# Kernel tuning notes

Hardware: AMD Instinct MI355X
Metric: run time of the kernel (lower is better)

The kernel has to match this reference:

```python
import jax, jax.numpy as jnp
import numpy as np

N_NODES = 500_000
N_EDGES = 32_000_000
D_COEF = 1.0  # 'd' init arg, constant


def setup_inputs() -> dict:
    key = jax.random.key(0)
    k1, k2, k3 = jax.random.split(key, 3)
    theta = jax.random.normal(k1, (N_NODES, 1), dtype=jnp.float32)
    src = jax.random.randint(k2, (N_EDGES,), 0, N_NODES, dtype=jnp.int32)
    dst = jax.random.randint(k3, (N_EDGES,), 0, N_NODES, dtype=jnp.int32)
    logc = jnp.asarray(np.log(1.5), dtype=jnp.float32)  # continuousTimeVicsek2D.logc
    u0 = jnp.asarray(0.3, dtype=jnp.float32)
    return {"theta": theta, "logc": logc, "u0": u0, "src": src, "dst": dst}


def reference(theta, logc, u0, src, dst):
    # calc_message: dtheta = theta[src] - theta[dst]; m = exp(logc)*sin(d*dtheta)
    dtheta = theta[src] - theta[dst]              # [E,1] edge gather
    msg = jnp.exp(logc) * jnp.sin(dtheta * D_COEF)  # [E,1]
    # aggregate_message: mean over each node's incoming mailbox (segment mean by dst)
    n = theta.shape[0]
    w_sum = jax.ops.segment_sum(msg, dst, num_segments=n)          # [N,1]
    cnt = jax.ops.segment_sum(jnp.ones((dst.shape[0], 1), msg.dtype), dst, num_segments=n)
    w = w_sum / jnp.maximum(cnt, 1.0)             # [N,1] torque (0 if no in-edges)
    # polarity2velocity: v = u0 * [cos(theta), sin(theta)]
    v = u0 * jnp.concatenate([jnp.cos(theta), jnp.sin(theta)], axis=-1)  # [N,2]
    # return torque and velocity concatenated: [N,3] = [w | v]
    return jnp.concatenate([w, v], axis=-1)
```

## Files before the change

### kernel.cpp

```cpp
#include <hip/hip_runtime.h>


#define NB 62
#define BSHIFT 13
#define NODES_PER_B 8192
#define CAPB 548000u
#define TPB 256
#define EPT 16
#define EPI (TPB * EPT)
#define K_SLICES 8
#define MSG_BITS 18

__global__ __launch_bounds__(TPB) void scatter_kernel(
    const float* __restrict__ theta,
    const float* __restrict__ logc,
    const int* __restrict__ src,
    const int* __restrict__ dst,
    unsigned int* __restrict__ recs,
    unsigned int* __restrict__ cursors,
    int n_edges, int n_iters)
{
    __shared__ unsigned int hist[NB];
    __shared__ unsigned int rankc[NB];
    __shared__ unsigned int offs[NB];
    __shared__ unsigned int gbase[NB];
    __shared__ unsigned int sbuf[EPI];
    __shared__ unsigned char sbkt[EPI];

    const float c = __expf(logc[0]);
    const int tid = threadIdx.x;

    for (int iter = blockIdx.x; iter < n_iters; iter += gridDim.x) {
        const int base = iter * EPI + tid * EPT;

        if (tid < NB) { hist[tid] = 0; rankc[tid] = 0; }
        __syncthreads();

        unsigned int myrec[EPT];
        int myb[EPT];

        if (base + EPT <= n_edges) {
            int4 s4[4], d4[4];
            #pragma unroll
            for (int q = 0; q < 4; ++q) {
                s4[q] = ((const int4*)(src + base))[q];
                d4[q] = ((const int4*)(dst + base))[q];
            }
            const int* sp = (const int*)s4;
            const int* dp = (const int*)d4;
            #pragma unroll
            for (int j = 0; j < EPT; ++j) {
                int dn = dp[j];
                float m = c * __sinf(theta[sp[j]] - theta[dn]);
                unsigned int a18 = (unsigned int)((m + 2.0f) * 65536.0f + 0.5f);
                myrec[j] = (((unsigned int)(dn & (NODES_PER_B - 1))) << MSG_BITS) | a18;
                int b = dn >> BSHIFT;
                myb[j] = b;
                atomicAdd(&hist[b], 1u);
            }
        } else {
            #pragma unroll
            for (int j = 0; j < EPT; ++j) {
                int e = base + j;
                if (e < n_edges) {
                    int dn = dst[e];
                    float m = c * __sinf(theta[src[e]] - theta[dn]);
                    unsigned int a18 = (unsigned int)((m + 2.0f) * 65536.0f + 0.5f);
                    myrec[j] = (((unsigned int)(dn & (NODES_PER_B - 1))) << MSG_BITS) | a18;
                    int b = dn >> BSHIFT;
                    myb[j] = b;
                    atomicAdd(&hist[b], 1u);
                } else {
                    myb[j] = -1;
                }
            }
        }
        __syncthreads();

        if (tid < 64) {
            unsigned int h = (tid < NB) ? hist[tid] : 0u;
            unsigned int x = h;
            #pragma unroll
            for (int dlt = 1; dlt < 64; dlt <<= 1) {
                unsigned int y = __shfl_up(x, dlt, 64);
                if (tid >= dlt) x += y;
            }
            if (tid < NB) {
                offs[tid] = x - h;
                gbase[tid] = h ? atomicAdd(&cursors[tid], h) : 0u;
            }
        }
        __syncthreads();

        #pragma unroll
        for (int j = 0; j < EPT; ++j) {
            int b = myb[j];
            if (b >= 0) {
                unsigned int r = atomicAdd(&rankc[b], 1u);
                unsigned int slot = offs[b] + r;
                sbuf[slot] = myrec[j];
                sbkt[slot] = (unsigned char)b;
            }
        }
        __syncthreads();

        unsigned int total = offs[NB - 1] + hist[NB - 1];
        for (unsigned int slot = tid; slot < total; slot += TPB) {
            unsigned int b = sbkt[slot];
            unsigned int gpos = gbase[b] + (slot - offs[b]);
            if (gpos < CAPB) recs[(size_t)b * CAPB + gpos] = sbuf[slot];
        }
        __syncthreads();
    }
}

__global__ __launch_bounds__(TPB) void reduce_kernel(
    const unsigned int* __restrict__ recs,
    const unsigned int* __restrict__ cursors,
    unsigned int* __restrict__ partials)
{
    __shared__ unsigned int acc[NODES_PER_B];
    const int tid = threadIdx.x;
    const int b = blockIdx.x >> 3;
    const int k = blockIdx.x & 7;

    for (int j = tid; j < NODES_PER_B; j += TPB) acc[j] = 0u;
    __syncthreads();

    unsigned int cnt = cursors[b];
    if (cnt > CAPB) cnt = CAPB;
    unsigned int slice = (cnt + K_SLICES - 1) / K_SLICES;
    unsigned int lo = (unsigned int)k * slice;
    unsigned int hi = lo + slice; if (hi > cnt) hi = cnt;

    const unsigned int* bp = recs + (size_t)b * CAPB;
    unsigned int i = lo + tid;
    for (; i + 3u * TPB < hi; i += 4u * TPB) {
        unsigned int r0 = bp[i];
        unsigned int r1 = bp[i + TPB];
        unsigned int r2 = bp[i + 2u * TPB];
        unsigned int r3 = bp[i + 3u * TPB];
        unsigned int a0 = ((r0 & 0x3FFFFu) + 2u) >> 2;
        unsigned int a1 = ((r1 & 0x3FFFFu) + 2u) >> 2;
        unsigned int a2 = ((r2 & 0x3FFFFu) + 2u) >> 2;
        unsigned int a3 = ((r3 & 0x3FFFFu) + 2u) >> 2;
        atomicAdd(&acc[r0 >> MSG_BITS], (a0 << 8) | 1u);
        atomicAdd(&acc[r1 >> MSG_BITS], (a1 << 8) | 1u);
        atomicAdd(&acc[r2 >> MSG_BITS], (a2 << 8) | 1u);
        atomicAdd(&acc[r3 >> MSG_BITS], (a3 << 8) | 1u);
    }
    for (; i < hi; i += TPB) {
        unsigned int rec = bp[i];
        unsigned int a = ((rec & 0x3FFFFu) + 2u) >> 2;
        atomicAdd(&acc[rec >> MSG_BITS], (a << 8) | 1u);
    }
    __syncthreads();

    unsigned int* pb = partials + (size_t)blockIdx.x * NODES_PER_B;
    for (int j = tid; j < NODES_PER_B; j += TPB) pb[j] = acc[j];
}

__global__ __launch_bounds__(TPB) void node_kernel(
    const float* __restrict__ theta,
    const float* __restrict__ u0p,
    const unsigned int* __restrict__ partials,
    float* __restrict__ out,
    int n_nodes)
{
    int i = blockIdx.x * TPB + threadIdx.x;
    if (i >= n_nodes) return;
    int b = i >> BSHIFT;
    int l = i & (NODES_PER_B - 1);

    unsigned int cnt = 0; int sum = 0;
    #pragma unroll
    for (int k = 0; k < K_SLICES; ++k) {
        unsigned int p = partials[(size_t)(b * K_SLICES + k) * NODES_PER_B + l];
        cnt += p & 255u;
        sum += (int)(p >> 8);
    }
    int net = sum - (int)cnt * 32768;
    float w = (float)net * (1.0f / 16384.0f) / fmaxf((float)cnt, 1.0f);

    float t = theta[i];
    float u0 = u0p[0];
    out[3 * i + 0] = w;
    out[3 * i + 1] = u0 * __cosf(t);
    out[3 * i + 2] = u0 * __sinf(t);
}

__global__ __launch_bounds__(256) void edge_kernel_fb(
    const float* __restrict__ theta, const float* __restrict__ logc,
    const int* __restrict__ src, const int* __restrict__ dst,
    unsigned long long* __restrict__ acc, int n_edges)
{
    const float c = __expf(logc[0]);
    int base = (blockIdx.x * 256 + threadIdx.x) * 4;
    if (base + 3 < n_edges) {
        int4 s4 = *(const int4*)(src + base);
        int4 d4 = *(const int4*)(dst + base);
        float m0 = c * __sinf(theta[s4.x] - theta[d4.x]);
        float m1 = c * __sinf(theta[s4.y] - theta[d4.y]);
        float m2 = c * __sinf(theta[s4.z] - theta[d4.z]);
        float m3 = c * __sinf(theta[s4.w] - theta[d4.w]);
        atomicAdd(&acc[d4.x], ((unsigned long long)((m0 + 2.0f) * 1073741824.0f) << 24) | 1ull);
        atomicAdd(&acc[d4.y], ((unsigned long long)((m1 + 2.0f) * 1073741824.0f) << 24) | 1ull);
        atomicAdd(&acc[d4.z], ((unsigned long long)((m2 + 2.0f) * 1073741824.0f) << 24) | 1ull);
        atomicAdd(&acc[d4.w], ((unsigned long long)((m3 + 2.0f) * 1073741824.0f) << 24) | 1ull);
    } else {
        for (int e = base; e < n_edges; ++e) {
            int s = src[e], d = dst[e];
            float m = c * __sinf(theta[s] - theta[d]);
            atomicAdd(&acc[d], ((unsigned long long)((m + 2.0f) * 1073741824.0f) << 24) | 1ull);
        }
    }
}

__global__ __launch_bounds__(256) void node_kernel_fb(
    const float* __restrict__ theta, const float* __restrict__ u0p,
    const unsigned long long* __restrict__ acc, float* __restrict__ out, int n_nodes)
{
    int i = blockIdx.x * 256 + threadIdx.x;
    if (i >= n_nodes) return;
    unsigned long long p = acc[i];
    long long cnt = (long long)(p & 0xFFFFFFull);
    long long net = (long long)(p >> 24) - (cnt << 31);
    float sum = (float)((double)net * (1.0 / 1073741824.0));
    float w = sum / fmaxf((float)cnt, 1.0f);
    float t = theta[i]; float u0 = u0p[0];
    out[3 * i + 0] = w;
    out[3 * i + 1] = u0 * __cosf(t);
    out[3 * i + 2] = u0 * __sinf(t);
}

extern "C" void kernel_launch(void* const* d_in, const int* in_sizes, int n_in,
                              void* d_out, int out_size, void* d_ws, size_t ws_size,
                              hipStream_t stream) {
    const float* theta = (const float*)d_in[0];
    const float* logc  = (const float*)d_in[1];
    const float* u0    = (const float*)d_in[2];
    const int*   src   = (const int*)d_in[3];
    const int*   dst   = (const int*)d_in[4];
    float* out = (float*)d_out;

    int n_nodes = in_sizes[0];
    int n_edges = in_sizes[3];

    size_t recs_bytes     = (size_t)NB * CAPB * sizeof(unsigned int);
    size_t cursors_off    = (recs_bytes + 255) & ~(size_t)255;
    size_t partials_off   = (cursors_off + 256 + 255) & ~(size_t)255;
    size_t partials_bytes = (size_t)NB * K_SLICES * NODES_PER_B * sizeof(unsigned int);
    size_t need = partials_off + partials_bytes;

    bool fast = (ws_size >= need) && (n_nodes <= NB * NODES_PER_B);

    if (fast) {
        unsigned int* recs     = (unsigned int*)d_ws;
        unsigned int* cursors  = (unsigned int*)((char*)d_ws + cursors_off);
        unsigned int* partials = (unsigned int*)((char*)d_ws + partials_off);

        hipMemsetAsync(cursors, 0, 256, stream);

        int n_iters = (n_edges + EPI - 1) / EPI;
        scatter_kernel<<<n_iters, TPB, 0, stream>>>(theta, logc, src, dst,
                                                    recs, cursors, n_edges, n_iters);

        reduce_kernel<<<NB * K_SLICES, TPB, 0, stream>>>(recs, cursors, partials);

        int nblocks = (n_nodes + TPB - 1) / TPB;
        node_kernel<<<nblocks, TPB, 0, stream>>>(theta, u0, partials, out, n_nodes);
    } else {
        unsigned long long* acc = (unsigned long long*)d_ws;
        hipMemsetAsync(d_ws, 0, (size_t)n_nodes * sizeof(unsigned long long), stream);
        int eblocks = (n_edges + 1023) / 1024;
        edge_kernel_fb<<<eblocks, 256, 0, stream>>>(theta, logc, src, dst, acc, n_edges);
        int nblocks = (n_nodes + 255) / 256;
        node_kernel_fb<<<nblocks, 256, 0, stream>>>(theta, u0, acc, out, n_nodes);
    }
}
```

Measured before the change: 566.4 us.

## Defer message computation to reduce kernel using shared-memory dst theta

The scatter kernel no longer gathers theta or computes sin. It packs the raw source index (19 bits) with the local destination index into each record. The reduce kernel stages the bucket's destination thetas in shared memory, gathers theta[src] from global memory, and computes and quantizes the message there. This replaces the random global theta[dst] gather with LDS reads. The block size of the reduce kernel is also raised to 512. The quantization scale changes slightly (16384 applied directly instead of 65536 then a shift), and the fast path now requires n_nodes to fit in 19 bits.

```diff
diff --git a/kernel.cpp b/kernel.cpp
--- a/kernel.cpp
+++ b/kernel.cpp
@@ -9,11 +9,11 @@
 #define EPT 16
 #define EPI (TPB * EPT)
 #define K_SLICES 8
-#define MSG_BITS 18
+#define SRC_BITS 19
+#define SRC_MASK 0x7FFFFu
+#define TPB_R 512
 
 __global__ __launch_bounds__(TPB) void scatter_kernel(
-    const float* __restrict__ theta,
-    const float* __restrict__ logc,
     const int* __restrict__ src,
     const int* __restrict__ dst,
     unsigned int* __restrict__ recs,
@@ -27,7 +27,6 @@
     __shared__ unsigned int sbuf[EPI];
     __shared__ unsigned char sbkt[EPI];
 
-    const float c = __expf(logc[0]);
     const int tid = threadIdx.x;
 
     for (int iter = blockIdx.x; iter < n_iters; iter += gridDim.x) {
@@ -51,9 +50,8 @@
             #pragma unroll
             for (int j = 0; j < EPT; ++j) {
                 int dn = dp[j];
-                float m = c * __sinf(theta[sp[j]] - theta[dn]);
-                unsigned int a18 = (unsigned int)((m + 2.0f) * 65536.0f + 0.5f);
-                myrec[j] = (((unsigned int)(dn & (NODES_PER_B - 1))) << MSG_BITS) | a18;
+                myrec[j] = (((unsigned int)(dn & (NODES_PER_B - 1))) << SRC_BITS)
+                         | (unsigned int)sp[j];
                 int b = dn >> BSHIFT;
                 myb[j] = b;
                 atomicAdd(&hist[b], 1u);
@@ -64,9 +62,8 @@
                 int e = base + j;
                 if (e < n_edges) {
                     int dn = dst[e];
-                    float m = c * __sinf(theta[src[e]] - theta[dn]);
-                    unsigned int a18 = (unsigned int)((m + 2.0f) * 65536.0f + 0.5f);
-                    myrec[j] = (((unsigned int)(dn & (NODES_PER_B - 1))) << MSG_BITS) | a18;
+                    myrec[j] = (((unsigned int)(dn & (NODES_PER_B - 1))) << SRC_BITS)
+                             | (unsigned int)src[e];
                     int b = dn >> BSHIFT;
                     myb[j] = b;
                     atomicAdd(&hist[b], 1u);
@@ -114,17 +111,27 @@
     }
 }
 
-__global__ __launch_bounds__(TPB) void reduce_kernel(
+__global__ __launch_bounds__(TPB_R, 4) void reduce_kernel(
+    const float* __restrict__ theta,
+    const float* __restrict__ logc,
     const unsigned int* __restrict__ recs,
     const unsigned int* __restrict__ cursors,
-    unsigned int* __restrict__ partials)
-{
+    unsigned int* __restrict__ partials,
+    int n_nodes)
+{
+    __shared__ float thd[NODES_PER_B];
     __shared__ unsigned int acc[NODES_PER_B];
     const int tid = threadIdx.x;
     const int b = blockIdx.x >> 3;
     const int k = blockIdx.x & 7;
-
-    for (int j = tid; j < NODES_PER_B; j += TPB) acc[j] = 0u;
+    const float c = __expf(logc[0]);
+    const int nbase = b * NODES_PER_B;
+
+    for (int j = tid; j < NODES_PER_B; j += TPB_R) {
+        int g = nbase + j;
+        thd[j] = (g < n_nodes) ? theta[g] : 0.0f;
+        acc[j] = 0u;
+    }
     __syncthreads();
 
     unsigned int cnt = cursors[b];
@@ -135,29 +142,42 @@
 
     const unsigned int* bp = recs + (size_t)b * CAPB;
     unsigned int i = lo + tid;
-    for (; i + 3u * TPB < hi; i += 4u * TPB) {
+    for (; i + 3u * TPB_R < hi; i += 4u * TPB_R) {
         unsigned int r0 = bp[i];
-        unsigned int r1 = bp[i + TPB];
-        unsigned int r2 = bp[i + 2u * TPB];
-        unsigned int r3 = bp[i + 3u * TPB];
-        unsigned int a0 = ((r0 & 0x3FFFFu) + 2u) >> 2;
-        unsigned int a1 = ((r1 & 0x3FFFFu) + 2u) >> 2;
-        unsigned int a2 = ((r2 & 0x3FFFFu) + 2u) >> 2;
-        unsigned int a3 = ((r3 & 0x3FFFFu) + 2u) >> 2;
-        atomicAdd(&acc[r0 >> MSG_BITS], (a0 << 8) | 1u);
-        atomicAdd(&acc[r1 >> MSG_BITS], (a1 << 8) | 1u);
-        atomicAdd(&acc[r2 >> MSG_BITS], (a2 << 8) | 1u);
-        atomicAdd(&acc[r3 >> MSG_BITS], (a3 << 8) | 1u);
-    }
-    for (; i < hi; i += TPB) {
+        unsigned int r1 = bp[i + TPB_R];
+        unsigned int r2 = bp[i + 2u * TPB_R];
+        unsigned int r3 = bp[i + 3u * TPB_R];
+        float s0 = theta[r0 & SRC_MASK];
+        float s1 = theta[r1 & SRC_MASK];
+        float s2 = theta[r2 & SRC_MASK];
+        float s3 = theta[r3 & SRC_MASK];
+        unsigned int l0 = r0 >> SRC_BITS, l1 = r1 >> SRC_BITS;
+        unsigned int l2 = r2 >> SRC_BITS, l3 = r3 >> SRC_BITS;
+        float m0 = c * __sinf(s0 - thd[l0]);
+        float m1 = c * __sinf(s1 - thd[l1]);
+        float m2 = c * __sinf(s2 - thd[l2]);
+        float m3 = c * __sinf(s3 - thd[l3]);
+        unsigned int a0 = (unsigned int)((m0 + 2.0f) * 16384.0f + 0.5f);
+        unsigned int a1 = (unsigned int)((m1 + 2.0f) * 16384.0f + 0.5f);
+        unsigned int a2 = (unsigned int)((m2 + 2.0f) * 16384.0f + 0.5f);
+        unsigned int a3 = (unsigned int)((m3 + 2.0f) * 16384.0f + 0.5f);
+        atomicAdd(&acc[l0], (a0 << 8) | 1u);
+        atomicAdd(&acc[l1], (a1 << 8) | 1u);
+        atomicAdd(&acc[l2], (a2 << 8) | 1u);
+        atomicAdd(&acc[l3], (a3 << 8) | 1u);
+    }
+    for (; i < hi; i += TPB_R) {
         unsigned int rec = bp[i];
-        unsigned int a = ((rec & 0x3FFFFu) + 2u) >> 2;
-        atomicAdd(&acc[rec >> MSG_BITS], (a << 8) | 1u);
+        float s = theta[rec & SRC_MASK];
+        unsigned int l = rec >> SRC_BITS;
+        float m = c * __sinf(s - thd[l]);
+        unsigned int a = (unsigned int)((m + 2.0f) * 16384.0f + 0.5f);
+        atomicAdd(&acc[l], (a << 8) | 1u);
     }
     __syncthreads();
 
     unsigned int* pb = partials + (size_t)blockIdx.x * NODES_PER_B;
-    for (int j = tid; j < NODES_PER_B; j += TPB) pb[j] = acc[j];
+    for (int j = tid; j < NODES_PER_B; j += TPB_R) pb[j] = acc[j];
 }
 
 __global__ __launch_bounds__(TPB) void node_kernel(
@@ -252,7 +272,8 @@
     size_t partials_bytes = (size_t)NB * K_SLICES * NODES_PER_B * sizeof(unsigned int);
     size_t need = partials_off + partials_bytes;
 
-    bool fast = (ws_size >= need) && (n_nodes <= NB * NODES_PER_B);
+    bool fast = (ws_size >= need) && (n_nodes <= NB * NODES_PER_B)
+                && (n_nodes <= (1 << SRC_BITS));
 
     if (fast) {
         unsigned int* recs     = (unsigned int*)d_ws;
@@ -262,10 +283,11 @@
         hipMemsetAsync(cursors, 0, 256, stream);
 
         int n_iters = (n_edges + EPI - 1) / EPI;
-        scatter_kernel<<<n_iters, TPB, 0, stream>>>(theta, logc, src, dst,
-                                                    recs, cursors, n_edges, n_iters);
-
-        reduce_kernel<<<NB * K_SLICES, TPB, 0, stream>>>(recs, cursors, partials);
+        scatter_kernel<<<n_iters, TPB, 0, stream>>>(src, dst, recs, cursors,
+                                                    n_edges, n_iters);
+
+        reduce_kernel<<<NB * K_SLICES, TPB_R, 0, stream>>>(theta, logc, recs,
+                                                           cursors, partials, n_nodes);
 
         int nblocks = (n_nodes + TPB - 1) / TPB;
         node_kernel<<<nblocks, TPB, 0, stream>>>(theta, u0, partials, out, n_nodes);
```

Measured after the change: 528.9 us. 6.6% less time.
